# Kernel optimization log

Hardware: AMD Instinct MI355X
Metric: run time of the kernel (lower is better)

Reference implementation:

```python
import jax, jax.numpy as jnp
import numpy as np

HEADS = 4
DIM_HEAD = 32


def setup_inputs() -> dict:
    key = jax.random.key(0)
    k1, k2, k3 = jax.random.split(key, 3)
    b, c, d, h, w = 2, 64, 48, 48, 48
    hidden = HEADS * DIM_HEAD  # 128
    x = jax.random.normal(k1, (b, c, d, h, w), dtype=jnp.float32)
    # 1x1x1 convs are pointwise linear maps over channels
    w_qkv = jax.random.normal(k2, (hidden * 3, c), dtype=jnp.float32) * (1.0 / np.sqrt(c))
    w_out = jax.random.normal(k3, (c, hidden), dtype=jnp.float32) * (1.0 / np.sqrt(hidden))
    b_out = jnp.zeros((c,), dtype=jnp.float32)
    return {"x": x, "w_qkv": w_qkv, "w_out": w_out, "b_out": b_out}


def reference(x, w_qkv, w_out, b_out):
    b, c, d, h, w = x.shape
    n = d * h * w
    xf = x.reshape(b, c, n)                                # [b,c,n]
    qkv = jnp.einsum('oc,bcn->bon', w_qkv, xf)             # [b,3*heads*dh,n]
    qkv = qkv.reshape(b, 3, HEADS, DIM_HEAD, n)            # split order: qkv, heads, c
    q, k, v = qkv[:, 0], qkv[:, 1], qkv[:, 2]              # each [b,heads,dh,n]
    k = jax.nn.softmax(k, axis=-1)
    context = jnp.einsum('bhdn,bhen->bhde', k, v)          # [b,heads,dh,dh]
    out = jnp.einsum('bhde,bhdn->bhen', context, q)        # [b,heads,dh,n]
    out = out.reshape(b, HEADS * DIM_HEAD, n)
    out = jnp.einsum('co,bon->bcn', w_out, out) + b_out[None, :, None]
    return out.reshape(b, c, d, h, w)
```

## Files before the change

### kernel.cpp

```cpp
#include <hip/hip_runtime.h>
#include <stdint.h>


using f32x4 = __attribute__((ext_vector_type(4))) float;
using s16x8 = __attribute__((ext_vector_type(8))) short;

#define NSP 110592
#define NSHADOW 16
#define MFMA(a, b, c) __builtin_amdgcn_mfma_f32_16x16x32_bf16((a), (b), (c), 0, 0, 0)

static __device__ __forceinline__ unsigned short f2bf(float f) {
    return (unsigned short)((__float_as_uint(f) + 0x8000u) >> 16);
}

__global__ __launch_bounds__(256, 4) void k1w(
    const float* __restrict__ x, const float* __restrict__ wqkv,
    float* __restrict__ Sdst, float* __restrict__ Zdst, int mode)
{
    __shared__ unsigned short XT[2][64][68];
    __shared__ unsigned short EKV[4][2][32][40];
    const int tid = threadIdx.x;
    const int wv = tid >> 6;
    const int l = tid & 63;
    const int l15 = l & 15, l4 = l >> 4;
    const int blk = blockIdx.x;
    const int b = blk / 432;
    const int tbase = (blk % 432) * 8;
    const int h = wv;

    s16x8 afr[2][2][2];
    for (int kv = 0; kv < 2; ++kv)
        for (int mt = 0; mt < 2; ++mt)
            for (int s = 0; s < 2; ++s) {
                int row = 128 + kv * 128 + h * 32 + mt * 16 + l15;
                const float* wp = wqkv + row * 64 + s * 32 + l4 * 8;
                s16x8 a;
#pragma unroll
                for (int j = 0; j < 8; ++j) a[j] = (short)f2bf(wp[j]);
                afr[kv][mt][s] = a;
            }

    f32x4 sacc[2][2] = {};
    float zrow[8] = {};

    unsigned short (*EK)[40] = EKV[wv][0];
    unsigned short (*EV)[40] = EKV[wv][1];
    const float* xb = x + (size_t)b * 64 * NSP;

    const int c0 = tid >> 3;
    const int ng0 = (tid & 7) ^ (c0 & 7);
    const int c1 = (tid + 256) >> 3;
    const int ng1 = ((tid + 256) & 7) ^ (c1 & 7);

    float4 g0, g1;
    {
        const int n0 = tbase * 32;
        g0 = *(const float4*)(xb + (size_t)c0 * NSP + n0 + 4 * ng0);
        g1 = *(const float4*)(xb + (size_t)c1 * NSP + n0 + 4 * ng1);
    }

    for (int it = 0; it < 8; ++it) {
        unsigned short (*XB)[68] = XT[it & 1];
        {
            ushort4 u;
            u.x = f2bf(g0.x); u.y = f2bf(g0.y); u.z = f2bf(g0.z); u.w = f2bf(g0.w);
            *(ushort4*)&XB[c0][4 * ng0] = u;
            u.x = f2bf(g1.x); u.y = f2bf(g1.y); u.z = f2bf(g1.z); u.w = f2bf(g1.w);
            *(ushort4*)&XB[c1][4 * ng1] = u;
        }
        if (it < 7) {
            const int n0 = (tbase + it + 1) * 32;
            g0 = *(const float4*)(xb + (size_t)c0 * NSP + n0 + 4 * ng0);
            g1 = *(const float4*)(xb + (size_t)c1 * NSP + n0 + 4 * ng1);
        }
        __syncthreads();

        f32x4 ck[2][2] = {}, cv[2][2] = {};
#pragma unroll
        for (int s = 0; s < 2; ++s)
#pragma unroll
            for (int nt = 0; nt < 2; ++nt) {
                s16x8 bfr;
#pragma unroll
                for (int j = 0; j < 8; ++j)
                    bfr[j] = (short)XB[s * 32 + l4 * 8 + j][nt * 16 + l15];
#pragma unroll
                for (int mt = 0; mt < 2; ++mt) {
                    ck[mt][nt] = MFMA(afr[0][mt][s], bfr, ck[mt][nt]);
                    cv[mt][nt] = MFMA(afr[1][mt][s], bfr, cv[mt][nt]);
                }
            }
#pragma unroll
        for (int mt = 0; mt < 2; ++mt)
#pragma unroll
            for (int nt = 0; nt < 2; ++nt) {
                int col = nt * 16 + l15;
#pragma unroll
                for (int r = 0; r < 4; ++r) {
                    int row = mt * 16 + l4 * 4 + r;
                    float ek = __expf(ck[mt][nt][r]);
                    zrow[mt * 4 + r] += ek;
                    EK[row][col] = f2bf(ek);
                    EV[row][col] = f2bf(cv[mt][nt][r]);
                }
            }
#pragma unroll
        for (int td = 0; td < 2; ++td) {
            s16x8 a2 = *(const s16x8*)&EK[td * 16 + l15][l4 * 8];
#pragma unroll
            for (int te = 0; te < 2; ++te) {
                s16x8 b2 = *(const s16x8*)&EV[te * 16 + l15][l4 * 8];
                sacc[td][te] = MFMA(a2, b2, sacc[td][te]);
            }
        }
    }

#pragma unroll
    for (int i = 0; i < 8; ++i) {
        float z = zrow[i];
        z += __shfl_xor(z, 1);
        z += __shfl_xor(z, 2);
        z += __shfl_xor(z, 4);
        z += __shfl_xor(z, 8);
        zrow[i] = z;
    }

    if (mode == 0) {
        float* Zb = Zdst + (size_t)blk * 128;
        if (l15 == 0)
#pragma unroll
            for (int mt = 0; mt < 2; ++mt)
#pragma unroll
                for (int r = 0; r < 4; ++r)
                    Zb[h * 32 + mt * 16 + l4 * 4 + r] = zrow[mt * 4 + r];
        float* Sb = Sdst + (size_t)blk * 4096 + h * 1024;
#pragma unroll
        for (int td = 0; td < 2; ++td)
#pragma unroll
            for (int te = 0; te < 2; ++te)
#pragma unroll
                for (int r = 0; r < 4; ++r)
                    Sb[(td * 16 + l4 * 4 + r) * 32 + te * 16 + l15] =
                        sacc[td][te][r];
    } else {
        const int shadow = blk & (NSHADOW - 1);
        float* Zb = Zdst + (size_t)(shadow * 2 + b) * 128;
        if (l15 == 0)
#pragma unroll
            for (int mt = 0; mt < 2; ++mt)
#pragma unroll
                for (int r = 0; r < 4; ++r)
                    atomicAdd(&Zb[h * 32 + mt * 16 + l4 * 4 + r], zrow[mt * 4 + r]);
        float* Sb = Sdst + (size_t)(shadow * 2 + b) * 4096 + h * 1024;
#pragma unroll
        for (int td = 0; td < 2; ++td)
#pragma unroll
            for (int te = 0; te < 2; ++te)
#pragma unroll
                for (int r = 0; r < 4; ++r)
                    atomicAdd(&Sb[(td * 16 + l4 * 4 + r) * 32 + te * 16 + l15],
                              sacc[td][te][r]);
    }
}

__global__ __launch_bounds__(256) void k2pre(
    const float* __restrict__ Sp, const float* __restrict__ Zp,
    float* __restrict__ Ssh, float* __restrict__ Zsh)
{
    const int q = blockIdx.x & 3;
    const int b = (blockIdx.x >> 2) & 1;
    const int s = blockIdx.x >> 3;
    const int t = threadIdx.x;
    const int i = q * 1024 + t * 4;
    float4 acc = {0.f, 0.f, 0.f, 0.f};
#pragma unroll
    for (int j = 0; j < 27; ++j) {
        const float4 v =
            *(const float4*)&Sp[(size_t)(b * 432 + s + 16 * j) * 4096 + i];
        acc.x += v.x; acc.y += v.y; acc.z += v.z; acc.w += v.w;
    }
    *(float4*)&Ssh[(size_t)(s * 2 + b) * 4096 + i] = acc;
    if (q == 0 && t < 128) {
        float z = 0.f;
#pragma unroll
        for (int j = 0; j < 27; ++j)
            z += Zp[(size_t)(b * 432 + s + 16 * j) * 128 + t];
        Zsh[(size_t)(s * 2 + b) * 128 + t] = z;
    }
}

__global__ __launch_bounds__(1024) void k2s(
    const float* __restrict__ Ssh, const float* __restrict__ Zsh,
    const float* __restrict__ wout, const float* __restrict__ wqkv,
    unsigned short* __restrict__ WE)
{
    __shared__ float ctx[4][32][32];
    __shared__ float P[64][128];
    __shared__ float Zl[128];
    const int b = blockIdx.x;
    const int t = threadIdx.x;
    if (t < 128) {
        float z = 0.f;
#pragma unroll
        for (int s = 0; s < NSHADOW; ++s) z += Zsh[(size_t)(s * 2 + b) * 128 + t];
        Zl[t] = z;
    }
    __syncthreads();
    for (int i = t; i < 4096; i += 1024) {
        float sv = 0.f;
#pragma unroll
        for (int s = 0; s < NSHADOW; ++s) sv += Ssh[(size_t)(s * 2 + b) * 4096 + i];
        int h = i >> 10, d = (i >> 5) & 31;
        ctx[h][d][i & 31] = sv / Zl[h * 32 + d];
    }
    __syncthreads();
    for (int i = t; i < 8192; i += 1024) {
        int c = i >> 7, hd = i & 127, h = hd >> 5, d = hd & 31;
        const float* wo = wout + c * 128 + h * 32;
        float acc = 0.f;
#pragma unroll 8
        for (int e = 0; e < 32; ++e) acc += wo[e] * ctx[h][d][e];
        P[c][hd] = acc;
    }
    __syncthreads();
    for (int i = t; i < 4096; i += 1024) {
        int c = i >> 6, c2 = i & 63;
        float acc = 0.f;
#pragma unroll 8
        for (int hd = 0; hd < 128; ++hd) acc += P[c][hd] * wqkv[hd * 64 + c2];
        WE[b * 4096 + c * 64 + c2] = f2bf(acc);
    }
}

__global__ __launch_bounds__(256) void k3e(
    const float* __restrict__ x, const unsigned short* __restrict__ WE,
    const float* __restrict__ bout, float* __restrict__ out)
{
    const int tid = threadIdx.x;
    const int wv = tid >> 6;
    const int l = tid & 63;
    const int l15 = l & 15, l4 = l >> 4;
    const int b = blockIdx.x / 864;
    const int n0 = (blockIdx.x % 864) * 128;

    s16x8 afr[4][2];
#pragma unroll
    for (int mt = 0; mt < 4; ++mt)
#pragma unroll
        for (int s = 0; s < 2; ++s)
            afr[mt][s] = *(const s16x8*)(WE + b * 4096 + (mt * 16 + l15) * 64 + s * 32 + l4 * 8);

    float bias[4][4];
#pragma unroll
    for (int mt = 0; mt < 4; ++mt)
#pragma unroll
        for (int r = 0; r < 4; ++r) bias[mt][r] = bout[mt * 16 + l4 * 4 + r];

    const float* xb = x + (size_t)b * 64 * NSP;
    float* ob = out + (size_t)b * 64 * NSP;

    const int nq = wv * 32;
    const float* xq = xb + (size_t)(l4 * 8) * NSP + n0 + nq + l15;

    f32x4 acc[4][2] = {};
#pragma unroll
    for (int s = 0; s < 2; ++s) {
        float t0[8], t1[8];
#pragma unroll
        for (int j = 0; j < 8; ++j) {
            const float* p = xq + (size_t)(s * 32 + j) * NSP;
            t0[j] = p[0];
            t1[j] = p[16];
        }
        s16x8 b0, b1;
#pragma unroll
        for (int j = 0; j < 8; ++j) {
            b0[j] = (short)f2bf(t0[j]);
            b1[j] = (short)f2bf(t1[j]);
        }
#pragma unroll
        for (int mt = 0; mt < 4; ++mt) {
            acc[mt][0] = MFMA(afr[mt][s], b0, acc[mt][0]);
            acc[mt][1] = MFMA(afr[mt][s], b1, acc[mt][1]);
        }
    }

#pragma unroll
    for (int mt = 0; mt < 4; ++mt)
#pragma unroll
        for (int nt = 0; nt < 2; ++nt)
#pragma unroll
            for (int r = 0; r < 4; ++r)
                ob[(size_t)(mt * 16 + l4 * 4 + r) * NSP + n0 + nq + nt * 16 + l15] =
                    acc[mt][nt][r] + bias[mt][r];
}

extern "C" void kernel_launch(void* const* d_in, const int* in_sizes, int n_in,
                              void* d_out, int out_size, void* d_ws, size_t ws_size,
                              hipStream_t stream) {
    const float *x = nullptr, *wqkv = nullptr, *wout = nullptr, *bout = nullptr;
    for (int i = 0; i < n_in; ++i) {
        if (in_sizes[i] == 2 * 64 * NSP) x = (const float*)d_in[i];
        else if (in_sizes[i] == 384 * 64) wqkv = (const float*)d_in[i];
        else if (in_sizes[i] == 64 * 128) wout = (const float*)d_in[i];
        else if (in_sizes[i] == 64) bout = (const float*)d_in[i];
    }
    if (!x) x = (const float*)d_in[0];
    if (!wqkv) wqkv = (const float*)d_in[1];
    if (!wout) wout = (const float*)d_in[2];
    if (!bout) bout = (const float*)d_in[3];
    float* out = (float*)d_out;

    const size_t NEED_BIG = 15155200;
    if (ws_size >= NEED_BIG) {
        float* Sp = (float*)d_ws;
        float* Zp = (float*)((char*)d_ws + 14155776);
        float* Ssh = (float*)((char*)d_ws + 14598144);
        float* Zsh = (float*)((char*)d_ws + 15122432);
        unsigned short* WE = (unsigned short*)((char*)d_ws + 15138816);
        hipLaunchKernelGGL(k1w, dim3(864), dim3(256), 0, stream, x, wqkv, Sp, Zp, 0);
        hipLaunchKernelGGL(k2pre, dim3(128), dim3(256), 0, stream, Sp, Zp, Ssh, Zsh);
        hipLaunchKernelGGL(k2s, dim3(2), dim3(1024), 0, stream, Ssh, Zsh, wout, wqkv, WE);
        hipLaunchKernelGGL(k3e, dim3(1728), dim3(256), 0, stream, x, WE, bout, out);
    } else {
        float* Ssh = (float*)d_ws;
        float* Zsh = (float*)((char*)d_ws + 524288);
        unsigned short* WE = (unsigned short*)((char*)d_ws + 540672);
        hipMemsetAsync(d_ws, 0, 540672, stream);
        hipLaunchKernelGGL(k1w, dim3(864), dim3(256), 0, stream, x, wqkv, Ssh, Zsh, 1);
        hipLaunchKernelGGL(k2s, dim3(2), dim3(1024), 0, stream, Ssh, Zsh, wout, wqkv, WE);
        hipLaunchKernelGGL(k3e, dim3(1728), dim3(256), 0, stream, x, WE, bout, out);
    }
}
```

Baseline: 175.4 us.

## Cache bf16 copy of x in pass one and read it in output pass

```diff
diff --git a/kernel.cpp b/kernel.cpp
--- a/kernel.cpp
+++ b/kernel.cpp
@@ -13,19 +13,20 @@
     return (unsigned short)((__float_as_uint(f) + 0x8000u) >> 16);
 }
 
-__global__ __launch_bounds__(256, 4) void k1w(
+__global__ __launch_bounds__(256, 5) void k1x(
     const float* __restrict__ x, const float* __restrict__ wqkv,
-    float* __restrict__ Sdst, float* __restrict__ Zdst, int mode)
+    float* __restrict__ Sdst, float* __restrict__ Zdst,
+    unsigned short* __restrict__ xbf, int mode)
 {
-    __shared__ unsigned short XT[2][64][68];
+    __shared__ unsigned short XT[64][68];
     __shared__ unsigned short EKV[4][2][32][40];
     const int tid = threadIdx.x;
     const int wv = tid >> 6;
     const int l = tid & 63;
     const int l15 = l & 15, l4 = l >> 4;
     const int blk = blockIdx.x;
-    const int b = blk / 432;
-    const int tbase = (blk % 432) * 8;
+    const int b = blk / 864;
+    const int tbase = (blk % 864) * 4;
     const int h = wv;
 
     s16x8 afr[2][2][2];
@@ -46,6 +47,7 @@
     unsigned short (*EK)[40] = EKV[wv][0];
     unsigned short (*EV)[40] = EKV[wv][1];
     const float* xb = x + (size_t)b * 64 * NSP;
+    unsigned short* xbfb = xbf ? xbf + (size_t)b * 64 * NSP : nullptr;
 
     const int c0 = tid >> 3;
     const int ng0 = (tid & 7) ^ (c0 & 7);
@@ -59,16 +61,21 @@
         g1 = *(const float4*)(xb + (size_t)c1 * NSP + n0 + 4 * ng1);
     }
 
-    for (int it = 0; it < 8; ++it) {
-        unsigned short (*XB)[68] = XT[it & 1];
+    for (int it = 0; it < 4; ++it) {
+        if (it > 0) __syncthreads();
         {
-            ushort4 u;
-            u.x = f2bf(g0.x); u.y = f2bf(g0.y); u.z = f2bf(g0.z); u.w = f2bf(g0.w);
-            *(ushort4*)&XB[c0][4 * ng0] = u;
-            u.x = f2bf(g1.x); u.y = f2bf(g1.y); u.z = f2bf(g1.z); u.w = f2bf(g1.w);
-            *(ushort4*)&XB[c1][4 * ng1] = u;
-        }
-        if (it < 7) {
+            ushort4 u0, u1;
+            u0.x = f2bf(g0.x); u0.y = f2bf(g0.y); u0.z = f2bf(g0.z); u0.w = f2bf(g0.w);
+            u1.x = f2bf(g1.x); u1.y = f2bf(g1.y); u1.z = f2bf(g1.z); u1.w = f2bf(g1.w);
+            *(ushort4*)&XT[c0][4 * ng0] = u0;
+            *(ushort4*)&XT[c1][4 * ng1] = u1;
+            if (xbfb) {
+                const int n0c = (tbase + it) * 32;
+                *(ushort4*)(xbfb + (size_t)c0 * NSP + n0c + 4 * ng0) = u0;
+                *(ushort4*)(xbfb + (size_t)c1 * NSP + n0c + 4 * ng1) = u1;
+            }
+        }
+        if (it < 3) {
             const int n0 = (tbase + it + 1) * 32;
             g0 = *(const float4*)(xb + (size_t)c0 * NSP + n0 + 4 * ng0);
             g1 = *(const float4*)(xb + (size_t)c1 * NSP + n0 + 4 * ng1);
@@ -83,7 +90,7 @@
                 s16x8 bfr;
 #pragma unroll
                 for (int j = 0; j < 8; ++j)
-                    bfr[j] = (short)XB[s * 32 + l4 * 8 + j][nt * 16 + l15];
+                    bfr[j] = (short)XT[s * 32 + l4 * 8 + j][nt * 16 + l15];
 #pragma unroll
                 for (int mt = 0; mt < 2; ++mt) {
                     ck[mt][nt] = MFMA(afr[0][mt][s], bfr, ck[mt][nt]);
@@ -173,18 +180,18 @@
     const int t = threadIdx.x;
     const int i = q * 1024 + t * 4;
     float4 acc = {0.f, 0.f, 0.f, 0.f};
-#pragma unroll
-    for (int j = 0; j < 27; ++j) {
+#pragma unroll 6
+    for (int j = 0; j < 54; ++j) {
         const float4 v =
-            *(const float4*)&Sp[(size_t)(b * 432 + s + 16 * j) * 4096 + i];
+            *(const float4*)&Sp[(size_t)(b * 864 + s + 16 * j) * 4096 + i];
         acc.x += v.x; acc.y += v.y; acc.z += v.z; acc.w += v.w;
     }
     *(float4*)&Ssh[(size_t)(s * 2 + b) * 4096 + i] = acc;
     if (q == 0 && t < 128) {
         float z = 0.f;
-#pragma unroll
-        for (int j = 0; j < 27; ++j)
-            z += Zp[(size_t)(b * 432 + s + 16 * j) * 128 + t];
+#pragma unroll 6
+        for (int j = 0; j < 54; ++j)
+            z += Zp[(size_t)(b * 864 + s + 16 * j) * 128 + t];
         Zsh[(size_t)(s * 2 + b) * 128 + t] = z;
     }
 }
@@ -232,6 +239,63 @@
     }
 }
 
+__global__ __launch_bounds__(256) void k3f(
+    const unsigned short* __restrict__ xbf, const unsigned short* __restrict__ WE,
+    const float* __restrict__ bout, float* __restrict__ out)
+{
+    const int tid = threadIdx.x;
+    const int wv = tid >> 6;
+    const int l = tid & 63;
+    const int l15 = l & 15, l4 = l >> 4;
+    const int b = blockIdx.x / 864;
+    const int n0 = (blockIdx.x % 864) * 128;
+
+    s16x8 afr[4][2];
+#pragma unroll
+    for (int mt = 0; mt < 4; ++mt)
+#pragma unroll
+        for (int s = 0; s < 2; ++s)
+            afr[mt][s] = *(const s16x8*)(WE + b * 4096 + (mt * 16 + l15) * 64 + s * 32 + l4 * 8);
+
+    float bias[4][4];
+#pragma unroll
+    for (int mt = 0; mt < 4; ++mt)
+#pragma unroll
+        for (int r = 0; r < 4; ++r) bias[mt][r] = bout[mt * 16 + l4 * 4 + r];
+
+    const unsigned short* xbfb = xbf + (size_t)b * 64 * NSP;
+    float* ob = out + (size_t)b * 64 * NSP;
+
+    const int nq = wv * 32;
+    const unsigned short* xq = xbfb + (size_t)(l4 * 8) * NSP + n0 + nq + l15;
+
+    f32x4 acc[4][2] = {};
+#pragma unroll
+    for (int s = 0; s < 2; ++s) {
+        s16x8 b0, b1;
+#pragma unroll
+        for (int j = 0; j < 8; ++j) {
+            const unsigned short* p = xq + (size_t)(s * 32 + j) * NSP;
+            b0[j] = (short)p[0];
+            b1[j] = (short)p[16];
+        }
+#pragma unroll
+        for (int mt = 0; mt < 4; ++mt) {
+            acc[mt][0] = MFMA(afr[mt][s], b0, acc[mt][0]);
+            acc[mt][1] = MFMA(afr[mt][s], b1, acc[mt][1]);
+        }
+    }
+
+#pragma unroll
+    for (int mt = 0; mt < 4; ++mt)
+#pragma unroll
+        for (int nt = 0; nt < 2; ++nt)
+#pragma unroll
+            for (int r = 0; r < 4; ++r)
+                ob[(size_t)(mt * 16 + l4 * 4 + r) * NSP + n0 + nq + nt * 16 + l15] =
+                    acc[mt][nt][r] + bias[mt][r];
+}
+
 __global__ __launch_bounds__(256) void k3e(
     const float* __restrict__ x, const unsigned short* __restrict__ WE,
     const float* __restrict__ bout, float* __restrict__ out)
@@ -311,23 +375,25 @@
     if (!bout) bout = (const float*)d_in[3];
     float* out = (float*)d_out;
 
-    const size_t NEED_BIG = 15155200;
+    const size_t NEED_BIG = 58064896;
     if (ws_size >= NEED_BIG) {
         float* Sp = (float*)d_ws;
-        float* Zp = (float*)((char*)d_ws + 14155776);
-        float* Ssh = (float*)((char*)d_ws + 14598144);
-        float* Zsh = (float*)((char*)d_ws + 15122432);
-        unsigned short* WE = (unsigned short*)((char*)d_ws + 15138816);
-        hipLaunchKernelGGL(k1w, dim3(864), dim3(256), 0, stream, x, wqkv, Sp, Zp, 0);
+        float* Zp = (float*)((char*)d_ws + 28311552);
+        float* Ssh = (float*)((char*)d_ws + 29196288);
+        float* Zsh = (float*)((char*)d_ws + 29720576);
+        unsigned short* WE = (unsigned short*)((char*)d_ws + 29736960);
+        unsigned short* Xbf = (unsigned short*)((char*)d_ws + 29753344);
+        hipLaunchKernelGGL(k1x, dim3(1728), dim3(256), 0, stream, x, wqkv, Sp, Zp, Xbf, 0);
         hipLaunchKernelGGL(k2pre, dim3(128), dim3(256), 0, stream, Sp, Zp, Ssh, Zsh);
         hipLaunchKernelGGL(k2s, dim3(2), dim3(1024), 0, stream, Ssh, Zsh, wout, wqkv, WE);
-        hipLaunchKernelGGL(k3e, dim3(1728), dim3(256), 0, stream, x, WE, bout, out);
+        hipLaunchKernelGGL(k3f, dim3(1728), dim3(256), 0, stream, Xbf, WE, bout, out);
     } else {
         float* Ssh = (float*)d_ws;
         float* Zsh = (float*)((char*)d_ws + 524288);
         unsigned short* WE = (unsigned short*)((char*)d_ws + 540672);
         hipMemsetAsync(d_ws, 0, 540672, stream);
-        hipLaunchKernelGGL(k1w, dim3(864), dim3(256), 0, stream, x, wqkv, Ssh, Zsh, 1);
+        hipLaunchKernelGGL(k1x, dim3(1728), dim3(256), 0, stream, x, wqkv, Ssh, Zsh,
+                           (unsigned short*)nullptr, 1);
         hipLaunchKernelGGL(k2s, dim3(2), dim3(1024), 0, stream, Ssh, Zsh, wout, wqkv, WE);
         hipLaunchKernelGGL(k3e, dim3(1728), dim3(256), 0, stream, x, WE, bout, out);
     }
```

Result: slower. 259.5 us (+48.0%).
